# Kernel optimization log

Hardware: AMD Instinct MI355X
Metric: run time of the kernel (lower is better)

The kernel has to match this reference:

```python
import jax, jax.numpy as jnp
import numpy as np

B, N, T, D = 8, 64, 50, 4      # batch, atoms, timesteps, features per node
K, H = 2, 64                   # edge types, hidden (msg_hid = msg_out = n_hid)
START = 1                      # skip_first_edge_type=True
E = N * (N - 1)


def setup_inputs() -> dict:
    key = jax.random.key(0)
    ks = jax.random.split(key, 10)
    # fully-connected relation graph: all ordered pairs i != j
    recv_idx, send_idx = np.where(~np.eye(N, dtype=bool))
    eye = np.eye(N, dtype=np.float32)
    rel_rec = jnp.asarray(eye[recv_idx])    # [E, N] one-hot receivers
    rel_send = jnp.asarray(eye[send_idx])   # [E, N] one-hot senders
    s = 0.1
    return {
        "inputs": jax.random.normal(ks[0], (B, N, T, D), jnp.float32),
        "rel_type": jax.random.uniform(ks[1], (B, 1, E, K), jnp.float32),
        "rel_rec": rel_rec,
        "rel_send": rel_send,
        "fc1_w": jax.random.normal(ks[2], (K, H, 2 * D), jnp.float32) * s,
        "fc1_b": jnp.zeros((K, H), jnp.float32),
        "fc2_w": jax.random.normal(ks[3], (K, H, H), jnp.float32) * s,
        "fc2_b": jnp.zeros((K, H), jnp.float32),
        "out1_w": jax.random.normal(ks[4], (H, D + H), jnp.float32) * s,
        "out1_b": jnp.zeros((H,), jnp.float32),
        "out2_w": jax.random.normal(ks[5], (H, H), jnp.float32) * s,
        "out2_b": jnp.zeros((H,), jnp.float32),
        "out3_w": jax.random.normal(ks[6], (D, H), jnp.float32) * s,
        "out3_b": jnp.zeros((D,), jnp.float32),
        "pred_steps": 1,
    }


def reference(inputs, rel_type, rel_rec, rel_send,
              fc1_w, fc1_b, fc2_w, fc2_b,
              out1_w, out1_b, out2_w, out2_b, out3_w, out3_b,
              pred_steps):
    assert pred_steps == 1
    x_in = jnp.swapaxes(inputs, 1, 2)  # [B, T, N, D]
    t = x_in.shape[1]
    # rel_type [B,1,E,K] -> expand over time
    rt = jnp.broadcast_to(rel_type, (rel_type.shape[0], t) + rel_type.shape[2:])

    # node2edge: gather receivers/senders via one-hot matmuls
    recv = jnp.einsum('en,btnd->bted', rel_rec, x_in)
    send = jnp.einsum('en,btnd->bted', rel_send, x_in)
    pre_msg = jnp.concatenate([recv, send], axis=-1)  # [B,T,E,2D]

    # per-edge-type MLP, masked by inferred edge prob, accumulated
    all_msgs = jnp.zeros(pre_msg.shape[:3] + (H,), pre_msg.dtype)
    for i in range(START, K):
        h = jax.nn.relu(jnp.einsum('bted,hd->bteh', pre_msg, fc1_w[i]) + fc1_b[i])
        m = jax.nn.relu(jnp.einsum('bteh,oh->bteo', h, fc2_w[i]) + fc2_b[i])
        all_msgs = all_msgs + m * rt[..., i:i + 1]

    # edge2node: scatter-accumulate to receivers via one-hot transpose matmul
    agg = jnp.einsum('en,bteh->btnh', rel_rec, all_msgs)  # [B,T,N,H]

    aug = jnp.concatenate([x_in, agg], axis=-1)           # [B,T,N,D+H]
    h = jax.nn.relu(jnp.einsum('btni,oi->btno', aug, out1_w) + out1_b)
    h = jax.nn.relu(jnp.einsum('btni,oi->btno', h, out2_w) + out2_b)
    delta = jnp.einsum('btni,oi->btno', h, out3_w) + out3_b
    x_tp1 = x_in + delta                                  # predict_delta=True

    pred_all = x_tp1[:, :t - 1]                           # [B,T-1,N,D]
    return jnp.swapaxes(pred_all, 1, 2)                   # [B,N,T-1,D]
```

## Files before the change

### kernel.cpp

```cpp
#include <hip/hip_runtime.h>


#define NB 8
#define NN 64
#define NT 50
#define NTO 49
#define ND 4
#define NE 4032

typedef _Float16 f16x8 __attribute__((ext_vector_type(8)));
typedef _Float16 f16x4 __attribute__((ext_vector_type(4)));
typedef _Float16 f16x2 __attribute__((ext_vector_type(2)));
typedef float f32x4 __attribute__((ext_vector_type(4)));
typedef float f32x2 __attribute__((ext_vector_type(2)));

union Frag8 { unsigned u[4]; f16x8 f; f16x2 h[4]; };

__device__ __forceinline__ unsigned pk16(float lo, float hi) {
  return __builtin_bit_cast(unsigned, __builtin_amdgcn_cvt_pkrtz(lo, hi));
}

#define MFMA16(A, B, C) __builtin_amdgcn_mfma_f32_16x16x32_f16((A), (B), (C), 0, 0, 0)

__global__ __launch_bounds__(256) void nri_fused_kernel(
    const float* __restrict__ inputs,
    const float* __restrict__ rel_type,
    const float* __restrict__ fc1_w,
    const float* __restrict__ fc1_b,
    const float* __restrict__ fc2_w,
    const float* __restrict__ fc2_b,
    const float* __restrict__ out1_w,
    const float* __restrict__ out1_b,
    const float* __restrict__ out2_w,
    const float* __restrict__ out2_b,
    const float* __restrict__ out3_w,
    const float* __restrict__ out3_b,
    float* __restrict__ out)
{
  __shared__ __align__(16) char smem[15872];
  _Float16* const Vh   = (_Float16*)(smem);
  _Float16* const H1L  = (_Float16*)(smem);
  _Float16* const H2L  = (_Float16*)(smem + 4608);
  _Float16* const Ph   = (_Float16*)(smem + 9216);
  _Float16* const Rl   = (_Float16*)(smem + 11264);
  float4*   const Xl   = (float4*)  (smem + 13312);
  _Float16* const AggL = (_Float16*)(smem + 13568);

  const int bid    = blockIdx.x;
  const int tile   = bid & 3;
  const int t      = (bid >> 2) % NTO;
  const int b      = bid / (4 * NTO);
  const int n_base = tile * 16;
  const int tid  = threadIdx.x;
  const int lane = tid & 63;
  const int w    = tid >> 6;
  const int q    = lane >> 4;
  const int r    = lane & 15;

  {
    const int k = lane;
    const float4 w1r = *(const float4*)(fc1_w + 512 + k * 8);
    const float4 w1s = *(const float4*)(fc1_w + 516 + k * 8);
    const float  b1k = fc1_b[64 + k];
#pragma unroll
    for (int ii = 0; ii < 16; ++ii) {
      const int i = ii * 4 + w;
      const float4 x = *(const float4*)(inputs + ((b * NN + i) * NT + t) * ND);
      Vh[i * 72 + k] = (_Float16)(w1s.x*x.x + w1s.y*x.y + w1s.z*x.z + w1s.w*x.w);
    }
#pragma unroll
    for (int ii = 0; ii < 4; ++ii) {
      const int i = ii * 4 + w;
      const float4 x = *(const float4*)(inputs + ((b * NN + n_base + i) * NT + t) * ND);
      Ph[i * 64 + k] = (_Float16)(b1k + w1r.x*x.x + w1r.y*x.y + w1r.z*x.z + w1r.w*x.w);
    }
  }
#pragma unroll
  for (int ii = 0; ii < 4; ++ii) {
    const int idx = ii * 256 + tid;
    const int i = idx >> 6, s = idx & 63;
    const int n = n_base + i;
    const float v = (s == n) ? 0.f
                  : rel_type[(b * NE + n * 63 + (s < n ? s : s - 1)) * 2 + 1];
    Rl[idx] = (_Float16)v;
  }
  if (tid < 16)
    Xl[tid] = *(const float4*)(inputs + ((b * NN + n_base + tid) * NT + t) * ND);

  Frag8 bfr[4][2];
  float b2l[4];
#pragma unroll
  for (int nt = 0; nt < 4; ++nt) {
    const int o = nt * 16 + r;
    b2l[nt] = fc2_b[64 + o];
#pragma unroll
    for (int ks = 0; ks < 2; ++ks) {
      const float* p = fc2_w + 4096 + o * 64 + ks * 32 + q * 8;
      const float4 c0 = *(const float4*)p;
      const float4 c1 = *(const float4*)(p + 4);
      bfr[nt][ks].u[0] = pk16(c0.x, c0.y);
      bfr[nt][ks].u[1] = pk16(c0.z, c0.w);
      bfr[nt][ks].u[2] = pk16(c1.x, c1.y);
      bfr[nt][ks].u[3] = pk16(c1.z, c1.w);
    }
  }
  __syncthreads();

#pragma unroll 1
  for (int np = 0; np < 4; ++np) {
    const int ni = w * 4 + np;
    Frag8 pa0, pa1;
    pa0.f = *(const f16x8*)(Ph + ni * 64 + q * 8);
    pa1.f = *(const f16x8*)(Ph + ni * 64 + 32 + q * 8);

    Frag8 va0, va1;
    {
      const _Float16* vp = Vh + r * 72 + q * 8;
      va0.f = *(const f16x8*)vp;
      va1.f = *(const f16x8*)(vp + 32);
    }

    float ag[4] = {0.f, 0.f, 0.f, 0.f};
#pragma unroll
    for (int st = 0; st < 4; ++st) {
      Frag8 nva0, nva1;
      if (st < 3) {
        const _Float16* vp = Vh + ((st + 1) * 16 + r) * 72 + q * 8;
        nva0.f = *(const f16x8*)vp;
        nva1.f = *(const f16x8*)(vp + 32);
      }

      const f16x4 rt4 = *(const f16x4*)(Rl + ni * 64 + st * 16 + q * 4);

      Frag8 a0, a1;
      const f16x2 z = {(_Float16)0.f, (_Float16)0.f};
#pragma unroll
      for (int j = 0; j < 4; ++j) {
        a0.h[j] = __builtin_elementwise_max((f16x2)(pa0.h[j] + va0.h[j]), z);
        a1.h[j] = __builtin_elementwise_max((f16x2)(pa1.h[j] + va1.h[j]), z);
      }

      __builtin_amdgcn_s_setprio(1);
      const f32x4 z4 = {0.f, 0.f, 0.f, 0.f};
#pragma unroll
      for (int nt = 0; nt < 4; ++nt) {
        f32x4 d = {b2l[nt], b2l[nt], b2l[nt], b2l[nt]};
        d = MFMA16(a0.f, bfr[nt][0].f, d);
        d = MFMA16(a1.f, bfr[nt][1].f, d);
        const f32x4 p = __builtin_elementwise_max(d, z4);
        float s = ag[nt];
        s += (float)rt4[0] * p[0];
        s += (float)rt4[1] * p[1];
        s += (float)rt4[2] * p[2];
        s += (float)rt4[3] * p[3];
        ag[nt] = s;
      }
      __builtin_amdgcn_s_setprio(0);

      va0 = nva0; va1 = nva1;
    }

#pragma unroll
    for (int nt = 0; nt < 4; ++nt) {
      float s = ag[nt];
      s += __shfl_xor(s, 16); s += __shfl_xor(s, 32);
      ag[nt] = s;
    }
    const float aval = (q == 0) ? ag[0] : (q == 1) ? ag[1] : (q == 2) ? ag[2] : ag[3];
    AggL[ni * 72 + lane] = (_Float16)aval;
  }

  const int o = w * 16 + r;
  Frag8 B1[2], B2[2];
#pragma unroll
  for (int ks = 0; ks < 2; ++ks) {
    const float* p1 = out1_w + o * 68 + 4 + ks * 32 + q * 8;
    const float4 c0 = *(const float4*)p1;
    const float4 c1 = *(const float4*)(p1 + 4);
    B1[ks].u[0] = pk16(c0.x, c0.y); B1[ks].u[1] = pk16(c0.z, c0.w);
    B1[ks].u[2] = pk16(c1.x, c1.y); B1[ks].u[3] = pk16(c1.z, c1.w);
    const float* p2 = out2_w + o * 64 + ks * 32 + q * 8;
    const float4 e0 = *(const float4*)p2;
    const float4 e1 = *(const float4*)(p2 + 4);
    B2[ks].u[0] = pk16(e0.x, e0.y); B2[ks].u[1] = pk16(e0.z, e0.w);
    B2[ks].u[2] = pk16(e1.x, e1.y); B2[ks].u[3] = pk16(e1.z, e1.w);
  }
  const float4 w1x = *(const float4*)(out1_w + o * 68);
  const float b1o = out1_b[o];
  const float b2o = out2_b[o];
  __syncthreads();

  {
    Frag8 A0, A1;
    A0.f = *(const f16x8*)(AggL + r * 72 + q * 8);
    A1.f = *(const f16x8*)(AggL + r * 72 + 32 + q * 8);
    f32x4 d = {b1o, b1o, b1o, b1o};
    d = MFMA16(A0.f, B1[0].f, d);
    d = MFMA16(A1.f, B1[1].f, d);
#pragma unroll
    for (int reg = 0; reg < 4; ++reg) {
      const int n = q * 4 + reg;
      const float4 x = Xl[n];
      const float hv = d[reg] + x.x*w1x.x + x.y*w1x.y + x.z*w1x.z + x.w*w1x.w;
      H1L[n * 72 + o] = (_Float16)fmaxf(hv, 0.f);
    }
  }
  __syncthreads();

  {
    Frag8 A0, A1;
    A0.f = *(const f16x8*)(H1L + r * 72 + q * 8);
    A1.f = *(const f16x8*)(H1L + r * 72 + 32 + q * 8);
    f32x4 d = {b2o, b2o, b2o, b2o};
    d = MFMA16(A0.f, B2[0].f, d);
    d = MFMA16(A1.f, B2[1].f, d);
#pragma unroll
    for (int reg = 0; reg < 4; ++reg) {
      const int n = q * 4 + reg;
      H2L[n * 72 + o] = (_Float16)fmaxf(d[reg], 0.f);
    }
  }
  __syncthreads();

  if (w == 0) {
    Frag8 B3[2];
#pragma unroll
    for (int ks = 0; ks < 2; ++ks) {
      const float* p3 = out3_w + (r & 3) * 64 + ks * 32 + q * 8;
      const float4 c0 = *(const float4*)p3;
      const float4 c1 = *(const float4*)(p3 + 4);
      B3[ks].u[0] = pk16(c0.x, c0.y); B3[ks].u[1] = pk16(c0.z, c0.w);
      B3[ks].u[2] = pk16(c1.x, c1.y); B3[ks].u[3] = pk16(c1.z, c1.w);
    }
    Frag8 A0, A1;
    A0.f = *(const f16x8*)(H2L + r * 72 + q * 8);
    A1.f = *(const f16x8*)(H2L + r * 72 + 32 + q * 8);
    const float b3o = out3_b[r & 3];
    f32x4 d = {b3o, b3o, b3o, b3o};
    d = MFMA16(A0.f, B3[0].f, d);
    d = MFMA16(A1.f, B3[1].f, d);
    if (r < 4) {
      const float* xf = (const float*)Xl;
#pragma unroll
      for (int reg = 0; reg < 4; ++reg) {
        const int n = q * 4 + reg;
        out[((b * NN + n_base + n) * NTO + t) * ND + r] = xf[n * 4 + r] + d[reg];
      }
    }
  }
}

extern "C" void kernel_launch(void* const* d_in, const int* in_sizes, int n_in,
                              void* d_out, int out_size, void* d_ws, size_t ws_size,
                              hipStream_t stream) {
  const float* inputs   = (const float*)d_in[0];
  const float* rel_type = (const float*)d_in[1];
  const float* fc1_w  = (const float*)d_in[4];
  const float* fc1_b  = (const float*)d_in[5];
  const float* fc2_w  = (const float*)d_in[6];
  const float* fc2_b  = (const float*)d_in[7];
  const float* out1_w = (const float*)d_in[8];
  const float* out1_b = (const float*)d_in[9];
  const float* out2_w = (const float*)d_in[10];
  const float* out2_b = (const float*)d_in[11];
  const float* out3_w = (const float*)d_in[12];
  const float* out3_b = (const float*)d_in[13];
  float* out = (float*)d_out;

  nri_fused_kernel<<<NB * NTO * 4, 256, 0, stream>>>(
      inputs, rel_type, fc1_w, fc1_b, fc2_w, fc2_b,
      out1_w, out1_b, out2_w, out2_b, out3_w, out3_b, out);
}
```

Measured before the change: 112.0 us.

## Split node MLP by rows per wave and replace block barriers with LDS fences

The output MLP over the 16 nodes of a tile is repartitioned so that each wave owns 4 node rows and computes all 64 output channels. Each layer's intermediate then stays in a wave-private LDS region, which lets two __syncthreads be replaced with a waitcnt fence. The MFMA M dimension is now mostly wasted, since rows r&3 are duplicated and only q==0 results are kept. Each wave also loads all weight fragments, which raises register pressure and redundant global loads.

```diff
diff --git a/kernel.cpp b/kernel.cpp
--- a/kernel.cpp
+++ b/kernel.cpp
@@ -18,6 +18,12 @@
 
 __device__ __forceinline__ unsigned pk16(float lo, float hi) {
   return __builtin_bit_cast(unsigned, __builtin_amdgcn_cvt_pkrtz(lo, hi));
+}
+
+__device__ __forceinline__ void lds_fence() {
+  __builtin_amdgcn_sched_barrier(0);
+  asm volatile("s_waitcnt lgkmcnt(0)" ::: "memory");
+  __builtin_amdgcn_sched_barrier(0);
 }
 
 #define MFMA16(A, B, C) __builtin_amdgcn_mfma_f32_16x16x32_f16((A), (B), (C), 0, 0, 0)
@@ -39,8 +45,6 @@
 {
   __shared__ __align__(16) char smem[15872];
   _Float16* const Vh   = (_Float16*)(smem);
-  _Float16* const H1L  = (_Float16*)(smem);
-  _Float16* const H2L  = (_Float16*)(smem + 4608);
   _Float16* const Ph   = (_Float16*)(smem + 9216);
   _Float16* const Rl   = (_Float16*)(smem + 11264);
   float4*   const Xl   = (float4*)  (smem + 13312);
@@ -170,80 +174,115 @@
     AggL[ni * 72 + lane] = (_Float16)aval;
   }
 
-  const int o = w * 16 + r;
-  Frag8 B1[2], B2[2];
-#pragma unroll
-  for (int ks = 0; ks < 2; ++ks) {
-    const float* p1 = out1_w + o * 68 + 4 + ks * 32 + q * 8;
-    const float4 c0 = *(const float4*)p1;
-    const float4 c1 = *(const float4*)(p1 + 4);
-    B1[ks].u[0] = pk16(c0.x, c0.y); B1[ks].u[1] = pk16(c0.z, c0.w);
-    B1[ks].u[2] = pk16(c1.x, c1.y); B1[ks].u[3] = pk16(c1.z, c1.w);
-    const float* p2 = out2_w + o * 64 + ks * 32 + q * 8;
-    const float4 e0 = *(const float4*)p2;
-    const float4 e1 = *(const float4*)(p2 + 4);
-    B2[ks].u[0] = pk16(e0.x, e0.y); B2[ks].u[1] = pk16(e0.z, e0.w);
-    B2[ks].u[2] = pk16(e1.x, e1.y); B2[ks].u[3] = pk16(e1.z, e1.w);
-  }
-  const float4 w1x = *(const float4*)(out1_w + o * 68);
-  const float b1o = out1_b[o];
-  const float b2o = out2_b[o];
   __syncthreads();
 
+  _Float16* const Reg = AggL + (w * 4) * 72;
+  const float* const xf = (const float*)Xl;
+
   {
+    Frag8 B1f[4][2]; float b1v[4]; float4 w1xv[4];
+#pragma unroll
+    for (int nt = 0; nt < 4; ++nt) {
+      const int o = nt * 16 + r;
+      b1v[nt]  = out1_b[o];
+      w1xv[nt] = *(const float4*)(out1_w + o * 68);
+#pragma unroll
+      for (int ks = 0; ks < 2; ++ks) {
+        const float* p1 = out1_w + o * 68 + 4 + ks * 32 + q * 8;
+        const float4 c0 = *(const float4*)p1;
+        const float4 c1 = *(const float4*)(p1 + 4);
+        B1f[nt][ks].u[0] = pk16(c0.x, c0.y); B1f[nt][ks].u[1] = pk16(c0.z, c0.w);
+        B1f[nt][ks].u[2] = pk16(c1.x, c1.y); B1f[nt][ks].u[3] = pk16(c1.z, c1.w);
+      }
+    }
     Frag8 A0, A1;
-    A0.f = *(const f16x8*)(AggL + r * 72 + q * 8);
-    A1.f = *(const f16x8*)(AggL + r * 72 + 32 + q * 8);
-    f32x4 d = {b1o, b1o, b1o, b1o};
-    d = MFMA16(A0.f, B1[0].f, d);
-    d = MFMA16(A1.f, B1[1].f, d);
-#pragma unroll
-    for (int reg = 0; reg < 4; ++reg) {
-      const int n = q * 4 + reg;
-      const float4 x = Xl[n];
-      const float hv = d[reg] + x.x*w1x.x + x.y*w1x.y + x.z*w1x.z + x.w*w1x.w;
-      H1L[n * 72 + o] = (_Float16)fmaxf(hv, 0.f);
-    }
-  }
-  __syncthreads();
+    A0.f = *(const f16x8*)(Reg + (r & 3) * 72 + q * 8);
+    A1.f = *(const f16x8*)(Reg + (r & 3) * 72 + 32 + q * 8);
+    f32x4 d0 = {b1v[0], b1v[0], b1v[0], b1v[0]};
+    f32x4 d1 = {b1v[1], b1v[1], b1v[1], b1v[1]};
+    f32x4 d2 = {b1v[2], b1v[2], b1v[2], b1v[2]};
+    f32x4 d3 = {b1v[3], b1v[3], b1v[3], b1v[3]};
+    d0 = MFMA16(A0.f, B1f[0][0].f, d0); d0 = MFMA16(A1.f, B1f[0][1].f, d0);
+    d1 = MFMA16(A0.f, B1f[1][0].f, d1); d1 = MFMA16(A1.f, B1f[1][1].f, d1);
+    d2 = MFMA16(A0.f, B1f[2][0].f, d2); d2 = MFMA16(A1.f, B1f[2][1].f, d2);
+    d3 = MFMA16(A0.f, B1f[3][0].f, d3); d3 = MFMA16(A1.f, B1f[3][1].f, d3);
+    if (q == 0) {
+#pragma unroll
+      for (int reg = 0; reg < 4; ++reg) {
+        const int n = w * 4 + reg;
+        const float4 x = Xl[n];
+        const float xv0 = x.x*w1xv[0].x + x.y*w1xv[0].y + x.z*w1xv[0].z + x.w*w1xv[0].w;
+        const float xv1 = x.x*w1xv[1].x + x.y*w1xv[1].y + x.z*w1xv[1].z + x.w*w1xv[1].w;
+        const float xv2 = x.x*w1xv[2].x + x.y*w1xv[2].y + x.z*w1xv[2].z + x.w*w1xv[2].w;
+        const float xv3 = x.x*w1xv[3].x + x.y*w1xv[3].y + x.z*w1xv[3].z + x.w*w1xv[3].w;
+        Reg[reg * 72 +  0 + r] = (_Float16)fmaxf(d0[reg] + xv0, 0.f);
+        Reg[reg * 72 + 16 + r] = (_Float16)fmaxf(d1[reg] + xv1, 0.f);
+        Reg[reg * 72 + 32 + r] = (_Float16)fmaxf(d2[reg] + xv2, 0.f);
+        Reg[reg * 72 + 48 + r] = (_Float16)fmaxf(d3[reg] + xv3, 0.f);
+      }
+    }
+  }
+  lds_fence();
 
   {
+    Frag8 B2f[4][2]; float b2v[4];
+#pragma unroll
+    for (int nt = 0; nt < 4; ++nt) {
+      const int o = nt * 16 + r;
+      b2v[nt] = out2_b[o];
+#pragma unroll
+      for (int ks = 0; ks < 2; ++ks) {
+        const float* p2 = out2_w + o * 64 + ks * 32 + q * 8;
+        const float4 e0 = *(const float4*)p2;
+        const float4 e1 = *(const float4*)(p2 + 4);
+        B2f[nt][ks].u[0] = pk16(e0.x, e0.y); B2f[nt][ks].u[1] = pk16(e0.z, e0.w);
+        B2f[nt][ks].u[2] = pk16(e1.x, e1.y); B2f[nt][ks].u[3] = pk16(e1.z, e1.w);
+      }
+    }
     Frag8 A0, A1;
-    A0.f = *(const f16x8*)(H1L + r * 72 + q * 8);
-    A1.f = *(const f16x8*)(H1L + r * 72 + 32 + q * 8);
-    f32x4 d = {b2o, b2o, b2o, b2o};
-    d = MFMA16(A0.f, B2[0].f, d);
-    d = MFMA16(A1.f, B2[1].f, d);
-#pragma unroll
-    for (int reg = 0; reg < 4; ++reg) {
-      const int n = q * 4 + reg;
-      H2L[n * 72 + o] = (_Float16)fmaxf(d[reg], 0.f);
-    }
-  }
-  __syncthreads();
-
-  if (w == 0) {
-    Frag8 B3[2];
+    A0.f = *(const f16x8*)(Reg + (r & 3) * 72 + q * 8);
+    A1.f = *(const f16x8*)(Reg + (r & 3) * 72 + 32 + q * 8);
+    f32x4 d0 = {b2v[0], b2v[0], b2v[0], b2v[0]};
+    f32x4 d1 = {b2v[1], b2v[1], b2v[1], b2v[1]};
+    f32x4 d2 = {b2v[2], b2v[2], b2v[2], b2v[2]};
+    f32x4 d3 = {b2v[3], b2v[3], b2v[3], b2v[3]};
+    d0 = MFMA16(A0.f, B2f[0][0].f, d0); d0 = MFMA16(A1.f, B2f[0][1].f, d0);
+    d1 = MFMA16(A0.f, B2f[1][0].f, d1); d1 = MFMA16(A1.f, B2f[1][1].f, d1);
+    d2 = MFMA16(A0.f, B2f[2][0].f, d2); d2 = MFMA16(A1.f, B2f[2][1].f, d2);
+    d3 = MFMA16(A0.f, B2f[3][0].f, d3); d3 = MFMA16(A1.f, B2f[3][1].f, d3);
+    if (q == 0) {
+#pragma unroll
+      for (int reg = 0; reg < 4; ++reg) {
+        Reg[reg * 72 +  0 + r] = (_Float16)fmaxf(d0[reg], 0.f);
+        Reg[reg * 72 + 16 + r] = (_Float16)fmaxf(d1[reg], 0.f);
+        Reg[reg * 72 + 32 + r] = (_Float16)fmaxf(d2[reg], 0.f);
+        Reg[reg * 72 + 48 + r] = (_Float16)fmaxf(d3[reg], 0.f);
+      }
+    }
+  }
+  lds_fence();
+
+  {
+    Frag8 B3f[2];
 #pragma unroll
     for (int ks = 0; ks < 2; ++ks) {
       const float* p3 = out3_w + (r & 3) * 64 + ks * 32 + q * 8;
       const float4 c0 = *(const float4*)p3;
       const float4 c1 = *(const float4*)(p3 + 4);
-      B3[ks].u[0] = pk16(c0.x, c0.y); B3[ks].u[1] = pk16(c0.z, c0.w);
-      B3[ks].u[2] = pk16(c1.x, c1.y); B3[ks].u[3] = pk16(c1.z, c1.w);
+      B3f[ks].u[0] = pk16(c0.x, c0.y); B3f[ks].u[1] = pk16(c0.z, c0.w);
+      B3f[ks].u[2] = pk16(c1.x, c1.y); B3f[ks].u[3] = pk16(c1.z, c1.w);
     }
     Frag8 A0, A1;
-    A0.f = *(const f16x8*)(H2L + r * 72 + q * 8);
-    A1.f = *(const f16x8*)(H2L + r * 72 + 32 + q * 8);
+    A0.f = *(const f16x8*)(Reg + (r & 3) * 72 + q * 8);
+    A1.f = *(const f16x8*)(Reg + (r & 3) * 72 + 32 + q * 8);
     const float b3o = out3_b[r & 3];
     f32x4 d = {b3o, b3o, b3o, b3o};
-    d = MFMA16(A0.f, B3[0].f, d);
-    d = MFMA16(A1.f, B3[1].f, d);
-    if (r < 4) {
-      const float* xf = (const float*)Xl;
+    d = MFMA16(A0.f, B3f[0].f, d);
+    d = MFMA16(A1.f, B3f[1].f, d);
+    if (q == 0 && r < 4) {
 #pragma unroll
       for (int reg = 0; reg < 4; ++reg) {
-        const int n = q * 4 + reg;
+        const int n = w * 4 + reg;
         out[((b * NN + n_base + n) * NTO + t) * ND + r] = xf[n * 4 + r] + d[reg];
       }
     }
```

After: 128.1 us. 14.3% more time.
